# Optimization experiments

Measured on AMD Instinct MI355X. Metric: run time of the kernel, lower is better.

## Reference

```python
import jax, jax.numpy as jnp
import numpy as np

NUM_TOTAL = 150000
NUM_USER = 50000
NUM_ITEM = NUM_TOTAL - NUM_USER
D = 128
SOC_L = 2
CO_L = 2
NEG = 10
R = 0.7
E_SOC = 1600000
E_CO = 3200000
B = 512
MAX_UI = 64
MAX_IU = 50
W = 32
HOP = 3


def _sage_lgcn(x, src, dst, w, n, layers):
    # SAGEConv with edge-softmax weights over destination (LGCN 'mean' option).
    m = jax.lax.stop_gradient(jax.ops.segment_max(w, dst, num_segments=n))
    e = jnp.exp(w - m[dst])
    s = jax.ops.segment_sum(e, dst, num_segments=n)
    alpha = e / (s[dst] + 1e-16)
    for _ in range(layers):
        x = jax.ops.segment_sum(alpha[:, None] * x[src], dst, num_segments=n)
    return x  # LGCN.forward returns the last conv output (not the averaged sum)


def _sym_lgcn(x, src, dst, n, layers):
    # LGCConv: gcn_norm with added self-loops, symmetric D^-1/2 A D^-1/2.
    loop = jnp.arange(n)
    s2 = jnp.concatenate([src, loop])
    d2 = jnp.concatenate([dst, loop])
    deg = jax.ops.segment_sum(jnp.ones_like(d2, dtype=jnp.float32), d2, num_segments=n)
    dinv = jnp.where(deg > 0, deg ** -0.5, 0.0)
    ew = dinv[s2] * dinv[d2]
    for _ in range(layers):
        x = jax.ops.segment_sum(ew[:, None] * x[s2], d2, num_segments=n)
    return x


def _l2norm(x):
    return x / jnp.maximum(jnp.linalg.norm(x, axis=-1, keepdims=True), 1e-12)


def setup_inputs() -> dict:
    ks = jax.random.split(jax.random.key(0), 10)
    id_emb = 0.1 * jax.random.normal(ks[0], (NUM_TOTAL, D), jnp.float32)
    soc_id_emb = 0.1 * jax.random.normal(ks[1], (NUM_TOTAL, D), jnp.float32)
    soc_ext_weight = jax.random.uniform(ks[2], (E_SOC,), jnp.float32)
    soc_edge_index = jax.random.randint(ks[3], (2, E_SOC), 0, NUM_TOTAL)
    co_edge_index = jax.random.randint(ks[4], (2, E_CO), 0, NUM_TOTAL)
    uid = jax.random.randint(ks[5], (B,), 0, NUM_USER)
    pi = jax.random.randint(ks[9], (B,), NUM_USER, NUM_TOTAL)
    n_id = jnp.stack([uid, pi], axis=1)
    user_items = jax.random.randint(ks[6], (B, MAX_UI), 0, NUM_ITEM)
    item_users = jax.random.randint(ks[7], (NUM_ITEM, MAX_IU), 0, NUM_USER)
    walks = jax.random.randint(ks[8], (B, W, HOP), 0, NUM_TOTAL)
    return dict(id_emb=id_emb, soc_id_emb=soc_id_emb, soc_ext_weight=soc_ext_weight,
                soc_edge_index=soc_edge_index, co_edge_index=co_edge_index, n_id=n_id,
                user_items=user_items, item_users=item_users, walks=walks)


def reference(id_emb, soc_id_emb, soc_ext_weight, soc_edge_index, co_edge_index,
              n_id, user_items, item_users, walks):
    pi_id = n_id[:, 1]
    # two message-passing stacks
    soc_emb = _sage_lgcn(soc_id_emb, soc_edge_index[0], soc_edge_index[1],
                         soc_ext_weight, NUM_TOTAL, SOC_L)
    co_emb = _sym_lgcn(id_emb, co_edge_index[0], co_edge_index[1], NUM_TOTAL, CO_L)
    zero = jnp.zeros((1, D), id_emb.dtype)
    co_pad = jnp.concatenate([co_emb, zero], 0)
    soc_pad = jnp.concatenate([soc_emb, zero], 0)
    # vectorized per-user negative sampling: exclude interacted items, sample
    # NEG without replacement via top-k over masked uniform noise.
    rows = jnp.arange(B)[:, None]
    cols = jnp.where(user_items >= 0, user_items, 0)
    avail = jnp.ones((B, NUM_ITEM), jnp.int32).at[rows, cols].min(
        (user_items < 0).astype(jnp.int32))
    noise = jax.random.uniform(jax.random.key(42), (B, NUM_ITEM))
    scorez = jnp.where(avail > 0, noise, -1.0)
    _, neg_local = jax.lax.top_k(scorez, NEG)
    cand = jnp.concatenate([pi_id[:, None], neg_local + NUM_USER], axis=1)  # [B, 1+NEG]
    # item anchor soc embedding = mean of soc_emb over interacting users
    iu_idx = jnp.where(item_users >= 0, item_users, NUM_TOTAL)  # pad -> zero row
    cnt = (item_users >= 0).sum(-1, keepdims=True).astype(id_emb.dtype) + 1e-7
    anchor = soc_pad[iu_idx].sum(1) / cnt  # [NUM_ITEM, D]
    u_ref = jnp.concatenate([soc_emb[:NUM_USER], anchor, zero], 0)  # [NUM_TOTAL+1, D]
    co_n = _l2norm(co_pad)
    soc_n = _l2norm(u_ref)
    wk = walks.reshape(B, -1)  # [B, W*HOP]
    co_sim = (jnp.einsum('bcd,bwd->bcw', co_n[cand], co_n[wk]) + 1.0) * 0.5
    soc_sim = (jnp.einsum('bcd,bwd->bcw', soc_n[cand], soc_n[wk]) + 1.0) * 0.5
    return R * co_sim.mean(-1) + (1.0 - R) * soc_sim.mean(-1)  # [B, 1+NEG]
```

## Files before the change

kernel.cpp:

```cpp
#include <hip/hip_runtime.h>
#include <hip/hip_fp16.h>
#include <stdint.h>

#define NUM_TOTAL 150000
#define NUM_USER  50000
#define NUM_ITEM  100000
#define E_SOC 1600000
#define E_CO  3200000
#define BATCH 512
#define MAX_UI 64
#define MAX_IU 50
#define NWALK 96
#define NCAND 11
#define NB    586
#define NWG   192
#define PARTS 4
#define PIT   25000
#define PMW   784
#define SCAP  192
#define TH    8377900u

__device__ __forceinline__ uint32_t rotl32(uint32_t x, int r){ return (x<<r)|(x>>(32-r)); }

__device__ __forceinline__ void tf_core(uint32_t x0, uint32_t x1, uint32_t& o0, uint32_t& o1){
  const uint32_t k0 = 0u, k1 = 42u, k2 = 0u ^ 42u ^ 0x1BD11BDAu;
  x0 += k0; x1 += k1;
#define TF_R4(a,b,c,d) \
  x0+=x1; x1=rotl32(x1,a); x1^=x0; \
  x0+=x1; x1=rotl32(x1,b); x1^=x0; \
  x0+=x1; x1=rotl32(x1,c); x1^=x0; \
  x0+=x1; x1=rotl32(x1,d); x1^=x0;
  TF_R4(13,15,26,6)   x0+=k1; x1+=k2+1u;
  TF_R4(17,29,16,24)  x0+=k2; x1+=k0+2u;
  TF_R4(13,15,26,6)   x0+=k0; x1+=k1+3u;
  TF_R4(17,29,16,24)  x0+=k1; x1+=k2+4u;
  TF_R4(13,15,26,6)   x0+=k2; x1+=k0+5u;
#undef TF_R4
  o0 = x0; o1 = x1;
}

__device__ __forceinline__ uint32_t tf_bits(uint32_t j){
  uint32_t o0, o1;
  tf_core(0u, j, o0, o1);
  return o0 ^ o1;
}

__global__ __launch_bounds__(256) void pcountB_k(const int* __restrict__ socDst,
                                                 const int* __restrict__ coDst,
                                                 int chunkS, int chunkC,
                                                 int* __restrict__ cntMatS,
                                                 int* __restrict__ cntMatC){
  __shared__ int h[NB];
  int tid = threadIdx.x;
  bool isSoc = blockIdx.x < NWG;
  int wg = isSoc ? blockIdx.x : blockIdx.x - NWG;
  const int* dst = isSoc ? socDst : coDst;
  int E = isSoc ? E_SOC : E_CO;
  int chunk = isSoc ? chunkS : chunkC;
  int* cntMat = isSoc ? cntMatS : cntMatC;
  for (int i=tid; i<NB; i+=256) h[i]=0;
  __syncthreads();
  int lo = wg*chunk, hi = lo+chunk; if (hi > E) hi = E;
  for (int i=lo+tid; i<hi; i+=256) atomicAdd(&h[dst[i]>>8], 1);
  __syncthreads();
  for (int i=tid; i<NB; i+=256) cntMat[wg*NB + i] = h[i];
}

__global__ __launch_bounds__(1024) void pscan2_k(int* __restrict__ cntMatS, int* __restrict__ cntMatC,
                                                 int* __restrict__ bbaseS, int* __restrict__ bbaseC){
  __shared__ int sa[1024];
  int tid = threadIdx.x;
  int* cntMat = blockIdx.x ? cntMatC : cntMatS;
  int* bbase  = blockIdx.x ? bbaseC  : bbaseS;
  int E       = blockIdx.x ? E_CO    : E_SOC;
  int tot = 0;
  if (tid < NB){
    for (int wg=0; wg<NWG; ++wg) tot += cntMat[wg*NB + tid];
  }
  sa[tid] = tot;
  __syncthreads();
  for (int s=1; s<1024; s<<=1){
    int v = (tid>=s)?sa[tid-s]:0;
    __syncthreads();
    sa[tid] += v;
    __syncthreads();
  }
  if (tid < NB){
    int base = sa[tid] - tot;
    bbase[tid] = base;
    int run = base;
    for (int wg=0; wg<NWG; ++wg){
      int c = cntMat[wg*NB + tid];
      cntMat[wg*NB + tid] = run;
      run += c;
    }
  }
  if (tid == 0) bbase[NB] = E;
}

__global__ __launch_bounds__(256) void pplaceB_k(const int* __restrict__ socSrc,
        const int* __restrict__ socDst, const float* __restrict__ socWgt,
        const int* __restrict__ coSrc,  const int* __restrict__ coDst,
        const int* __restrict__ cntMatS, const int* __restrict__ cntMatC,
        unsigned long long* __restrict__ recS, unsigned int* __restrict__ recC,
        int chunkS, int chunkC){
  __shared__ int curx[NB];
  int tid = threadIdx.x;
  bool isSoc = blockIdx.x < NWG;
  int wg = isSoc ? blockIdx.x : blockIdx.x - NWG;
  const int* offMat = isSoc ? cntMatS : cntMatC;
  for (int i=tid; i<NB; i+=256) curx[i] = offMat[wg*NB + i];
  __syncthreads();
  if (isSoc){
    int lo = wg*chunkS, hi = lo+chunkS; if (hi > E_SOC) hi = E_SOC;
    for (int i=lo+tid; i<hi; i+=256){
      int d = socDst[i];
      int p = atomicAdd(&curx[d>>8], 1);
      recS[p] = ((unsigned long long)__float_as_uint(socWgt[i])<<32)
              | (unsigned)(((d&255)<<18) | socSrc[i]);
    }
  } else {
    int lo = wg*chunkC, hi = lo+chunkC; if (hi > E_CO) hi = E_CO;
    for (int i=lo+tid; i<hi; i+=256){
      int d = coDst[i];
      int p = atomicAdd(&curx[d>>8], 1);
      recC[p] = (unsigned)(((d&255)<<18) | coSrc[i]);
    }
  }
}

__global__ __launch_bounds__(256) void cscB_k(const unsigned long long* __restrict__ recS,
    const unsigned int* __restrict__ recC,
    const int* __restrict__ bbaseS, const int* __restrict__ bbaseC,
    int* __restrict__ socOff, int* __restrict__ socSrcS, float* __restrict__ socWS,
    int* __restrict__ coOff, int* __restrict__ coSrcS, float* __restrict__ dinv){
  __shared__ int cnt[256], basex[256], curx[256];
  int tid = threadIdx.x;
  bool isSoc = blockIdx.x < NB;
  int b = isSoc ? blockIdx.x : blockIdx.x - NB;
  const int* bbase = isSoc ? bbaseS : bbaseC;
  int lo = bbase[b], hi = bbase[b+1];
  cnt[tid] = 0;
  __syncthreads();
  if (isSoc){
    for (int i = lo + tid; i < hi; i += 256)
      atomicAdd(&cnt[(((unsigned)recS[i]) >> 18) & 255], 1);
  } else {
    for (int i = lo + tid; i < hi; i += 256)
      atomicAdd(&cnt[(recC[i] >> 18) & 255], 1);
  }
  __syncthreads();
  int c = cnt[tid];
  basex[tid] = c; __syncthreads();
  for (int s=1; s<256; s<<=1){
    int t = (tid>=s)?basex[tid-s]:0; __syncthreads();
    basex[tid]+=t; __syncthreads();
  }
  int excl = basex[tid]-c;
  int node = b*256+tid;
  int* off = isSoc ? socOff : coOff;
  if (node <= NUM_TOTAL) off[node] = lo + excl;
  basex[tid] = excl; curx[tid] = 0;
  __syncthreads();
  if (isSoc){
    for (int i = lo + tid; i < hi; i += 256){
      unsigned long long r = recS[i];
      unsigned lw = (unsigned)r;
      int dl = (lw>>18)&255;
      int p = lo + basex[dl] + atomicAdd(&curx[dl],1);
      socSrcS[p] = lw & 0x3FFFF;
      socWS[p] = __uint_as_float((unsigned)(r>>32));
    }
    __syncthreads();
    if (node < NUM_TOTAL && c > 0){
      int e0 = lo + basex[tid], e1 = e0 + c;
      float m = -3.402823466e+38f;
      for (int e=e0; e<e1; ++e) m = fmaxf(m, socWS[e]);
      float s = 0.f;
      for (int e=e0; e<e1; ++e) s += expf(socWS[e] - m);
      float inv = 1.0f / (s + 1e-16f);
      for (int e=e0; e<e1; ++e) socWS[e] = expf(socWS[e] - m) * inv;
    }
  } else {
    for (int i = lo + tid; i < hi; i += 256){
      unsigned r = recC[i];
      int dl = (r>>18)&255;
      int p = lo + basex[dl] + atomicAdd(&curx[dl],1);
      coSrcS[p] = r & 0x3FFFF;
    }
    if (node < NUM_TOTAL) dinv[node] = 1.0f / sqrtf((float)(c + 1));
  }
}

__global__ void f2h2_k(const float4* __restrict__ a, uint2* __restrict__ oa,
                       const float4* __restrict__ b, uint2* __restrict__ ob, int n4){
  int i = blockIdx.x*blockDim.x+threadIdx.x, st = gridDim.x*blockDim.x;
  for (; i<n4; i+=st){
    float4 va = a[i], vb = b[i];
    __half2 l = __float22half2_rn(make_float2(va.x,va.y));
    __half2 h = __float22half2_rn(make_float2(va.z,va.w));
    uint2 u; u.x = *(unsigned*)&l; u.y = *(unsigned*)&h;
    oa[i] = u;
    l = __float22half2_rn(make_float2(vb.x,vb.y));
    h = __float22half2_rn(make_float2(vb.z,vb.w));
    u.x = *(unsigned*)&l; u.y = *(unsigned*)&h;
    ob[i] = u;
  }
}

__global__ void agg_soc8_k(const __half2* __restrict__ x, __half2* __restrict__ y,
                           const int* __restrict__ off, const int* __restrict__ srcS,
                           const float* __restrict__ wE, int n){
  int gw = (blockIdx.x*blockDim.x + threadIdx.x) >> 6;
  int lane = threadIdx.x & 63;
  if (gw >= n) return;
  float ax = 0.f, ay = 0.f;
  int e = off[gw], e1 = off[gw+1];
  for (; e + 8 <= e1; e += 8){
    int s0=srcS[e],s1=srcS[e+1],s2=srcS[e+2],s3=srcS[e+3];
    int s4=srcS[e+4],s5=srcS[e+5],s6=srcS[e+6],s7=srcS[e+7];
    float a0=wE[e],a1=wE[e+1],a2=wE[e+2],a3=wE[e+3];
    float a4=wE[e+4],a5=wE[e+5],a6=wE[e+6],a7=wE[e+7];
    __half2 h0=x[(size_t)s0*64+lane], h1=x[(size_t)s1*64+lane];
    __half2 h2=x[(size_t)s2*64+lane], h3=x[(size_t)s3*64+lane];
    __half2 h4=x[(size_t)s4*64+lane], h5=x[(size_t)s5*64+lane];
    __half2 h6=x[(size_t)s6*64+lane], h7=x[(size_t)s7*64+lane];
    float2 f0=__half22float2(h0), f1=__half22float2(h1), f2=__half22float2(h2), f3=__half22float2(h3);
    float2 f4=__half22float2(h4), f5=__half22float2(h5), f6=__half22float2(h6), f7=__half22float2(h7);
    ax += a0*f0.x + a1*f1.x + a2*f2.x + a3*f3.x + a4*f4.x + a5*f5.x + a6*f6.x + a7*f7.x;
    ay += a0*f0.y + a1*f1.y + a2*f2.y + a3*f3.y + a4*f4.y + a5*f5.y + a6*f6.y + a7*f7.y;
  }
  for (; e < e1; ++e){
    int s = srcS[e]; float a = wE[e];
    float2 f = __half22float2(x[(size_t)s*64 + lane]);
    ax += a*f.x; ay += a*f.y;
  }
  y[(size_t)gw*64 + lane] = __float22half2_rn(make_float2(ax, ay));
}

__global__ void agg_co8_k(const __half2* __restrict__ x, __half2* __restrict__ y,
                          const int* __restrict__ off, const int* __restrict__ srcS,
                          const float* __restrict__ dinv, int n){
  int gw = (blockIdx.x*blockDim.x + threadIdx.x) >> 6;
  int lane = threadIdx.x & 63;
  if (gw >= n) return;
  float dv = dinv[gw];
  float2 fs = __half22float2(x[(size_t)gw*64 + lane]);
  float ax = dv*dv*fs.x, ay = dv*dv*fs.y;
  int e = off[gw], e1 = off[gw+1];
  for (; e + 8 <= e1; e += 8){
    int s0=srcS[e],s1=srcS[e+1],s2=srcS[e+2],s3=srcS[e+3];
    int s4=srcS[e+4],s5=srcS[e+5],s6=srcS[e+6],s7=srcS[e+7];
    float a0=dinv[s0]*dv,a1=dinv[s1]*dv,a2=dinv[s2]*dv,a3=dinv[s3]*dv;
    float a4=dinv[s4]*dv,a5=dinv[s5]*dv,a6=dinv[s6]*dv,a7=dinv[s7]*dv;
    __half2 h0=x[(size_t)s0*64+lane], h1=x[(size_t)s1*64+lane];
    __half2 h2=x[(size_t)s2*64+lane], h3=x[(size_t)s3*64+lane];
    __half2 h4=x[(size_t)s4*64+lane], h5=x[(size_t)s5*64+lane];
    __half2 h6=x[(size_t)s6*64+lane], h7=x[(size_t)s7*64+lane];
    float2 f0=__half22float2(h0), f1=__half22float2(h1), f2=__half22float2(h2), f3=__half22float2(h3);
    float2 f4=__half22float2(h4), f5=__half22float2(h5), f6=__half22float2(h6), f7=__half22float2(h7);
    ax += a0*f0.x + a1*f1.x + a2*f2.x + a3*f3.x + a4*f4.x + a5*f5.x + a6*f6.x + a7*f7.x;
    ay += a0*f0.y + a1*f1.y + a2*f2.y + a3*f3.y + a4*f4.y + a5*f5.y + a6*f6.y + a7*f7.y;
  }
  for (; e < e1; ++e){
    int s = srcS[e]; float a = dinv[s]*dv;
    float2 f = __half22float2(x[(size_t)s*64 + lane]);
    ax += a*f.x; ay += a*f.y;
  }
  y[(size_t)gw*64 + lane] = __float22half2_rn(make_float2(ax, ay));
}

__global__ void norm_h_k(__half2* __restrict__ x, int n){
  int gw = (blockIdx.x*blockDim.x + threadIdx.x) >> 6;
  int lane = threadIdx.x & 63;
  if (gw >= n) return;
  __half2* p = x + (size_t)gw*64;
  float2 v = __half22float2(p[lane]);
  float ss = v.x*v.x + v.y*v.y;
  #pragma unroll
  for (int s=32; s; s>>=1) ss += __shfl_xor(ss, s, 64);
  float sc = 1.0f / fmaxf(sqrtf(ss), 1e-12f);
  p[lane] = __float22half2_rn(make_float2(v.x*sc, v.y*sc));
}

__global__ void postA_k(__half2* __restrict__ coE, const __half2* __restrict__ socE,
                        const int* __restrict__ item_users, __half2* __restrict__ anch){
  int gw = (blockIdx.x*blockDim.x + threadIdx.x) >> 6;
  int lane = threadIdx.x & 63;
  if (gw < NUM_TOTAL){
    __half2* p = coE + (size_t)gw*64;
    float2 v = __half22float2(p[lane]);
    float ss = v.x*v.x + v.y*v.y;
    #pragma unroll
    for (int s=32; s; s>>=1) ss += __shfl_xor(ss, s, 64);
    float sc = 1.0f / fmaxf(sqrtf(ss), 1e-12f);
    p[lane] = __float22half2_rn(make_float2(v.x*sc, v.y*sc));
  } else {
    int it = gw - NUM_TOTAL;
    if (it >= NUM_ITEM) return;
    const int* us = item_users + (size_t)it*MAX_IU;
    float ax = 0.f, ay = 0.f;
    for (int k=0; k<MAX_IU; k+=10){
      int u0=us[k],u1=us[k+1],u2=us[k+2],u3=us[k+3],u4=us[k+4];
      int u5=us[k+5],u6=us[k+6],u7=us[k+7],u8=us[k+8],u9=us[k+9];
      __half2 h0=socE[(size_t)u0*64+lane], h1=socE[(size_t)u1*64+lane];
      __half2 h2=socE[(size_t)u2*64+lane], h3=socE[(size_t)u3*64+lane];
      __half2 h4=socE[(size_t)u4*64+lane], h5=socE[(size_t)u5*64+lane];
      __half2 h6=socE[(size_t)u6*64+lane], h7=socE[(size_t)u7*64+lane];
      __half2 h8=socE[(size_t)u8*64+lane], h9=socE[(size_t)u9*64+lane];
      float2 f0=__half22float2(h0), f1=__half22float2(h1), f2=__half22float2(h2);
      float2 f3=__half22float2(h3), f4=__half22float2(h4), f5=__half22float2(h5);
      float2 f6=__half22float2(h6), f7=__half22float2(h7), f8=__half22float2(h8);
      float2 f9=__half22float2(h9);
      ax += f0.x+f1.x+f2.x+f3.x+f4.x+f5.x+f6.x+f7.x+f8.x+f9.x;
      ay += f0.y+f1.y+f2.y+f3.y+f4.y+f5.y+f6.y+f7.y+f8.y+f9.y;
    }
    const float inv = 1.0f / (50.0f + 1e-7f);
    ax *= inv; ay *= inv;
    float ss = ax*ax + ay*ay;
    #pragma unroll
    for (int s=32; s; s>>=1) ss += __shfl_xor(ss, s, 64);
    float sc = 1.0f / fmaxf(sqrtf(ss), 1e-12f);
    anch[(size_t)it*64 + lane] = __float22half2_rn(make_float2(ax*sc, ay*sc));
  }
}

__global__ __launch_bounds__(256) void negA_k(const int* __restrict__ user_items,
                                              unsigned long long* __restrict__ surv,
                                              int* __restrict__ scnt){
  __shared__ unsigned int mask[PMW];
  __shared__ int lcnt;
  int blk = blockIdx.x;
  int row = blk >> 2, part = blk & 3;
  int base = part * PIT;
  int tid = threadIdx.x;
  for (int i=tid; i<PMW; i+=256) mask[i] = 0u;
  if (tid == 0) lcnt = 0;
  __syncthreads();
  if (tid < MAX_UI){
    int it = user_items[row*MAX_UI + tid];
    if (it >= base && it < base + PIT){
      int li = it - base;
      atomicOr(&mask[li>>5], 1u << (li & 31));
    }
  }
  __syncthreads();
  unsigned jbase = (unsigned)row * 100000u + (unsigned)base;
  for (int k = tid; k < PIT; k += 1024){
    int i1 = k + 256, i2 = k + 512, i3 = k + 768;
    uint32_t b0 = tf_bits(jbase + (unsigned)k);
    uint32_t b1 = tf_bits(jbase + (unsigned)(i1 < PIT ? i1 : k));
    uint32_t b2 = tf_bits(jbase + (unsigned)(i2 < PIT ? i2 : k));
    uint32_t b3 = tf_bits(jbase + (unsigned)(i3 < PIT ? i3 : k));
    uint32_t v0 = b0 >> 9, v1 = b1 >> 9, v2 = b2 >> 9, v3 = b3 >> 9;
    if (v0 >= TH && !((mask[k>>5] >> (k&31)) & 1u)){
      int p = atomicAdd(&lcnt, 1);
      if (p < SCAP)
        surv[(size_t)blk*SCAP + p] = ((unsigned long long)v0 << 32) | (unsigned)(~(unsigned)(base + k));
    }
    if (i1 < PIT && v1 >= TH && !((mask[i1>>5] >> (i1&31)) & 1u)){
      int p = atomicAdd(&lcnt, 1);
      if (p < SCAP)
        surv[(size_t)blk*SCAP + p] = ((unsigned long long)v1 << 32) | (unsigned)(~(unsigned)(base + i1));
    }
    if (i2 < PIT && v2 >= TH && !((mask[i2>>5] >> (i2&31)) & 1u)){
      int p = atomicAdd(&lcnt, 1);
      if (p < SCAP)
        surv[(size_t)blk*SCAP + p] = ((unsigned long long)v2 << 32) | (unsigned)(~(unsigned)(base + i2));
    }
    if (i3 < PIT && v3 >= TH && !((mask[i3>>5] >> (i3&31)) & 1u)){
      int p = atomicAdd(&lcnt, 1);
      if (p < SCAP)
        surv[(size_t)blk*SCAP + p] = ((unsigned long long)v3 << 32) | (unsigned)(~(unsigned)(base + i3));
    }
  }
  __syncthreads();
  if (tid == 0) scnt[blk] = (lcnt < SCAP) ? lcnt : SCAP;
}

__global__ __launch_bounds__(256) void negB_k(const unsigned long long* __restrict__ surv,
                                              const int* __restrict__ scnt,
                                              const int* __restrict__ user_items,
                                              const int* __restrict__ n_id,
                                              int* __restrict__ cand){
  __shared__ unsigned long long keys[PARTS*SCAP];
  __shared__ unsigned long long red[256];
  __shared__ int cnts[PARTS];
  __shared__ int uix[MAX_UI];
  int b = blockIdx.x, tid = threadIdx.x;
  if (tid < PARTS) cnts[tid] = scnt[b*PARTS + tid];
  for (int i=tid; i<PARTS*SCAP; i+=256) keys[i] = 0ull;
  __syncthreads();
  int o0 = 0, o1 = cnts[0], o2 = o1 + cnts[1], o3 = o2 + cnts[2];
  int total = o3 + cnts[3];
  if (tid < cnts[0]) keys[o0 + tid] = surv[(size_t)(b*PARTS+0)*SCAP + tid];
  if (tid < cnts[1]) keys[o1 + tid] = surv[(size_t)(b*PARTS+1)*SCAP + tid];
  if (tid < cnts[2]) keys[o2 + tid] = surv[(size_t)(b*PARTS+2)*SCAP + tid];
  if (tid < cnts[3]) keys[o3 + tid] = surv[(size_t)(b*PARTS+3)*SCAP + tid];
  __syncthreads();
  if (total >= 10){
    for (int r=0; r<10; ++r){
      unsigned long long m = 0ull;
      for (int i=tid; i<PARTS*SCAP; i+=256){ unsigned long long v = keys[i]; if (v > m) m = v; }
      red[tid] = m; __syncthreads();
      for (int s=128; s>0; s>>=1){
        if (tid < s && red[tid+s] > red[tid]) red[tid] = red[tid+s];
        __syncthreads();
      }
      unsigned long long win = red[0];
      if (tid == 0)
        cand[b*NCAND + 1 + r] = NUM_USER + (int)(~(unsigned)(win & 0xffffffffull));
      for (int i=tid; i<PARTS*SCAP; i+=256) if (keys[i] == win) keys[i] = 0ull;
      __syncthreads();
    }
  } else {
    if (tid < MAX_UI) uix[tid] = user_items[b*MAX_UI + tid];
    __syncthreads();
    unsigned long long prev = ~0ull;
    for (int r=0; r<10; ++r){
      unsigned long long m = 0ull;
      for (int i=tid; i<NUM_ITEM; i+=256){
        bool msk = false;
        for (int j=0; j<MAX_UI; ++j) if (uix[j] == i) msk = true;
        if (msk) continue;
        uint32_t v = tf_bits((unsigned)b*100000u + (unsigned)i) >> 9;
        unsigned long long key = ((unsigned long long)v << 32) | (unsigned)(~(unsigned)i);
        if (key < prev && key > m) m = key;
      }
      red[tid] = m; __syncthreads();
      for (int s=128; s>0; s>>=1){
        if (tid < s && red[tid+s] > red[tid]) red[tid] = red[tid+s];
        __syncthreads();
      }
      unsigned long long win = red[0];
      prev = win;
      if (tid == 0)
        cand[b*NCAND + 1 + r] = NUM_USER + (int)(~(unsigned)(win & 0xffffffffull));
      __syncthreads();
    }
  }
  if (tid == 0) cand[b*NCAND] = n_id[b*2 + 1];
}

__global__ void sim_h_k(const __half2* __restrict__ coN, const __half2* __restrict__ socU,
                        const __half2* __restrict__ socI, const int* __restrict__ cand,
                        const int* __restrict__ walks, float* __restrict__ out){
  int b = blockIdx.x;
  int lane = threadIdx.x;
  float scx=0.f, scy=0.f, ssx=0.f, ssy=0.f;
  for (int w=0; w<NWALK; w+=4){
    int i0 = walks[b*NWALK + w],   i1 = walks[b*NWALK + w+1];
    int i2 = walks[b*NWALK + w+2], i3 = walks[b*NWALK + w+3];
    __half2 c0 = coN[(size_t)i0*64 + lane], c1 = coN[(size_t)i1*64 + lane];
    __half2 c2 = coN[(size_t)i2*64 + lane], c3 = coN[(size_t)i3*64 + lane];
    const __half2* p0 = (i0 < NUM_USER) ? socU + (size_t)i0*64 : socI + (size_t)(i0-NUM_USER)*64;
    const __half2* p1 = (i1 < NUM_USER) ? socU + (size_t)i1*64 : socI + (size_t)(i1-NUM_USER)*64;
    const __half2* p2 = (i2 < NUM_USER) ? socU + (size_t)i2*64 : socI + (size_t)(i2-NUM_USER)*64;
    const __half2* p3 = (i3 < NUM_USER) ? socU + (size_t)i3*64 : socI + (size_t)(i3-NUM_USER)*64;
    __half2 s0 = p0[lane], s1 = p1[lane], s2 = p2[lane], s3 = p3[lane];
    float2 fc0 = __half22float2(c0), fc1 = __half22float2(c1);
    float2 fc2 = __half22float2(c2), fc3 = __half22float2(c3);
    float2 fs0 = __half22float2(s0), fs1 = __half22float2(s1);
    float2 fs2 = __half22float2(s2), fs3 = __half22float2(s3);
    scx += fc0.x + fc1.x + fc2.x + fc3.x;
    scy += fc0.y + fc1.y + fc2.y + fc3.y;
    ssx += fs0.x + fs1.x + fs2.x + fs3.x;
    ssy += fs0.y + fs1.y + fs2.y + fs3.y;
  }
  for (int c=0; c<NCAND; ++c){
    int idx = cand[b*NCAND + c];
    float2 cv = __half22float2(coN[(size_t)idx*64 + lane]);
    float2 sv = __half22float2(socI[(size_t)(idx - NUM_USER)*64 + lane]);
    float dco = cv.x*scx + cv.y*scy;
    float dso = sv.x*ssx + sv.y*ssy;
    #pragma unroll
    for (int s=32; s; s>>=1){
      dco += __shfl_xor(dco, s, 64);
      dso += __shfl_xor(dso, s, 64);
    }
    if (lane == 0){
      float com = 0.5f + 0.5f*(dco / 96.0f);
      float som = 0.5f + 0.5f*(dso / 96.0f);
      out[b*NCAND + c] = 0.7f*com + 0.3f*som;
    }
  }
}

extern "C" void kernel_launch(void* const* d_in, const int* in_sizes, int n_in,
                              void* d_out, int out_size, void* d_ws, size_t ws_size,
                              hipStream_t stream){
  (void)in_sizes; (void)n_in; (void)out_size; (void)ws_size;
  const float* id_emb     = (const float*)d_in[0];
  const float* soc_id_emb = (const float*)d_in[1];
  const float* soc_w      = (const float*)d_in[2];
  const int*   soc_ei     = (const int*)d_in[3];
  const int*   co_ei      = (const int*)d_in[4];
  const int*   n_id       = (const int*)d_in[5];
  const int*   user_items = (const int*)d_in[6];
  const int*   item_users = (const int*)d_in[7];
  const int*   walks      = (const int*)d_in[8];
  float* out = (float*)d_out;

  char* w = (char*)d_ws;
  size_t cur = 0;
  auto take = [&](size_t bytes)->void*{
    void* p = w + cur;
    cur = (cur + bytes + 255) & ~(size_t)255;
    return p;
  };
  __half2* socId16 = (__half2*)take((size_t)NUM_TOTAL*64*4);
  __half2* id16    = (__half2*)take((size_t)NUM_TOTAL*64*4);
  __half2* t16     = (__half2*)take((size_t)NUM_TOTAL*64*4);
  __half2* soc16   = (__half2*)take((size_t)NUM_TOTAL*64*4);
  __half2* co16    = (__half2*)take((size_t)NUM_TOTAL*64*4);
  int*   socOff  = (int*)take((size_t)(NUM_TOTAL+1)*4);
  int*   coOff   = (int*)take((size_t)(NUM_TOTAL+1)*4);
  float* dinv    = (float*)take((size_t)NUM_TOTAL*4);
  int*   socSrcS = (int*)take((size_t)E_SOC*4);
  float* socWS   = (float*)take((size_t)E_SOC*4);
  int*   coSrcS  = (int*)take((size_t)E_CO*4);
  int*   cntMatS = (int*)take((size_t)NWG*NB*4);
  int*   cntMatC = (int*)take((size_t)NWG*NB*4);
  int*   bbaseS  = (int*)take((size_t)(NB+1)*4);
  int*   bbaseC  = (int*)take((size_t)(NB+1)*4);
  unsigned long long* surv = (unsigned long long*)take((size_t)BATCH*PARTS*SCAP*8);
  int*   scnt    = (int*)take((size_t)BATCH*PARTS*4);
  int*   cand    = (int*)take((size_t)BATCH*NCAND*4);

  unsigned long long* recS = (unsigned long long*)t16;
  unsigned int*       recC = (unsigned int*)((char*)t16 + (size_t)E_SOC*8);

  __half2* anch16 = socId16;

  const int T = 256;
  const int chunkS = (E_SOC + NWG - 1) / NWG;
  const int chunkC = (E_CO  + NWG - 1) / NWG;

  pcountB_k<<<2*NWG, T, 0, stream>>>(soc_ei + E_SOC, co_ei + E_CO, chunkS, chunkC, cntMatS, cntMatC);
  pscan2_k<<<2, 1024, 0, stream>>>(cntMatS, cntMatC, bbaseS, bbaseC);
  pplaceB_k<<<2*NWG, T, 0, stream>>>(soc_ei, soc_ei + E_SOC, soc_w,
                                     co_ei, co_ei + E_CO,
                                     cntMatS, cntMatC, recS, recC, chunkS, chunkC);
  cscB_k<<<2*NB, T, 0, stream>>>(recS, recC, bbaseS, bbaseC,
                                 socOff, socSrcS, socWS, coOff, coSrcS, dinv);

  negA_k<<<BATCH*PARTS, T, 0, stream>>>(user_items, surv, scnt);

  f2h2_k<<<2048, T, 0, stream>>>((const float4*)soc_id_emb, (uint2*)socId16,
                                 (const float4*)id_emb,     (uint2*)id16, NUM_TOTAL*32);

  int aggGrid = (NUM_TOTAL + 3) / 4;
  agg_soc8_k<<<aggGrid, T, 0, stream>>>(socId16, soc16, socOff, socSrcS, socWS, NUM_TOTAL);
  agg_soc8_k<<<aggGrid, T, 0, stream>>>(soc16,   t16,   socOff, socSrcS, socWS, NUM_TOTAL);
  agg_co8_k <<<aggGrid, T, 0, stream>>>(id16,    co16,  coOff,  coSrcS,  dinv,  NUM_TOTAL);
  agg_co8_k <<<aggGrid, T, 0, stream>>>(co16,    id16,  coOff,  coSrcS,  dinv,  NUM_TOTAL);

  __half2* socE = t16;
  __half2* coE  = id16;

  postA_k<<<(2*NUM_TOTAL - NUM_USER + 3)/4, T, 0, stream>>>(coE, socE, item_users, anch16);
  norm_h_k<<<(NUM_USER + 3)/4, T, 0, stream>>>(socE, NUM_USER);

  negB_k<<<BATCH, T, 0, stream>>>(surv, scnt, user_items, n_id, cand);
  sim_h_k<<<BATCH, 64, 0, stream>>>(coE, socE, anch16, cand, walks, out);
}
```

Baseline: 983.6 us.

## Parallelize bucket-offset scan across wavefronts and fuse negative sampling with fp16 conversion

The count matrix is transposed to a bucket-major layout. The serial per-thread scan over 192 workgroups in a 2-block kernel is replaced by three kernels: a wavefront-per-bucket total, a small block scan, and a wavefront-per-bucket prefix that writes placement offsets. Separately, the negative-candidate survivor kernel and the fp32-to-fp16 embedding conversion are merged into one launch so their blocks can run concurrently. This adds two extra launches for the scan and a heterogeneous fused kernel.

```diff
diff --git a/kernel.cpp b/kernel.cpp
--- a/kernel.cpp
+++ b/kernel.cpp
@@ -63,39 +63,64 @@
   int lo = wg*chunk, hi = lo+chunk; if (hi > E) hi = E;
   for (int i=lo+tid; i<hi; i+=256) atomicAdd(&h[dst[i]>>8], 1);
   __syncthreads();
-  for (int i=tid; i<NB; i+=256) cntMat[wg*NB + i] = h[i];
-}
-
-__global__ __launch_bounds__(1024) void pscan2_k(int* __restrict__ cntMatS, int* __restrict__ cntMatC,
+  for (int i=tid; i<NB; i+=256) cntMat[(size_t)i*NWG + wg] = h[i];
+}
+
+__global__ void btot2_k(const int* __restrict__ cntMatS, const int* __restrict__ cntMatC,
+                        int* __restrict__ totS, int* __restrict__ totC){
+  int g = (blockIdx.x*blockDim.x + threadIdx.x) >> 6;
+  int lane = threadIdx.x & 63;
+  if (g >= 2*NB) return;
+  bool isSoc = g < NB;
+  int b = isSoc ? g : g - NB;
+  const int* row = (isSoc ? cntMatS : cntMatC) + (size_t)b*NWG;
+  int s = row[lane*3] + row[lane*3+1] + row[lane*3+2];
+  #pragma unroll
+  for (int d=32; d; d>>=1) s += __shfl_xor(s, d, 64);
+  if (lane == 0) (isSoc ? totS : totC)[b] = s;
+}
+
+__global__ __launch_bounds__(1024) void bscan2_k(const int* __restrict__ totS, const int* __restrict__ totC,
                                                  int* __restrict__ bbaseS, int* __restrict__ bbaseC){
   __shared__ int sa[1024];
   int tid = threadIdx.x;
-  int* cntMat = blockIdx.x ? cntMatC : cntMatS;
-  int* bbase  = blockIdx.x ? bbaseC  : bbaseS;
-  int E       = blockIdx.x ? E_CO    : E_SOC;
-  int tot = 0;
-  if (tid < NB){
-    for (int wg=0; wg<NWG; ++wg) tot += cntMat[wg*NB + tid];
-  }
-  sa[tid] = tot;
+  const int* tot = blockIdx.x ? totC : totS;
+  int* bbase     = blockIdx.x ? bbaseC : bbaseS;
+  int E          = blockIdx.x ? E_CO   : E_SOC;
+  int v = (tid < NB) ? tot[tid] : 0;
+  sa[tid] = v;
   __syncthreads();
   for (int s=1; s<1024; s<<=1){
-    int v = (tid>=s)?sa[tid-s]:0;
-    __syncthreads();
-    sa[tid] += v;
-    __syncthreads();
-  }
-  if (tid < NB){
-    int base = sa[tid] - tot;
-    bbase[tid] = base;
-    int run = base;
-    for (int wg=0; wg<NWG; ++wg){
-      int c = cntMat[wg*NB + tid];
-      cntMat[wg*NB + tid] = run;
-      run += c;
-    }
-  }
+    int t = (tid>=s)?sa[tid-s]:0;
+    __syncthreads();
+    sa[tid] += t;
+    __syncthreads();
+  }
+  if (tid < NB) bbase[tid] = sa[tid] - v;
   if (tid == 0) bbase[NB] = E;
+}
+
+__global__ void wgpfx2_k(int* __restrict__ cntMatS, int* __restrict__ cntMatC,
+                         const int* __restrict__ bbaseS, const int* __restrict__ bbaseC){
+  int g = (blockIdx.x*blockDim.x + threadIdx.x) >> 6;
+  int lane = threadIdx.x & 63;
+  if (g >= 2*NB) return;
+  bool isSoc = g < NB;
+  int b = isSoc ? g : g - NB;
+  int* row = (isSoc ? cntMatS : cntMatC) + (size_t)b*NWG;
+  int base = (isSoc ? bbaseS : bbaseC)[b];
+  int v0 = row[lane*3], v1 = row[lane*3+1], v2 = row[lane*3+2];
+  int s = v0 + v1 + v2;
+  int x = s;
+  #pragma unroll
+  for (int d=1; d<64; d<<=1){
+    int t = __shfl_up(x, d, 64);
+    if (lane >= d) x += t;
+  }
+  int excl = x - s;
+  row[lane*3]   = base + excl;
+  row[lane*3+1] = base + excl + v0;
+  row[lane*3+2] = base + excl + v0 + v1;
 }
 
 __global__ __launch_bounds__(256) void pplaceB_k(const int* __restrict__ socSrc,
@@ -109,7 +134,7 @@
   bool isSoc = blockIdx.x < NWG;
   int wg = isSoc ? blockIdx.x : blockIdx.x - NWG;
   const int* offMat = isSoc ? cntMatS : cntMatC;
-  for (int i=tid; i<NB; i+=256) curx[i] = offMat[wg*NB + i];
+  for (int i=tid; i<NB; i+=256) curx[i] = offMat[(size_t)i*NWG + wg];
   __syncthreads();
   if (isSoc){
     int lo = wg*chunkS, hi = lo+chunkS; if (hi > E_SOC) hi = E_SOC;
@@ -192,19 +217,73 @@
   }
 }
 
-__global__ void f2h2_k(const float4* __restrict__ a, uint2* __restrict__ oa,
-                       const float4* __restrict__ b, uint2* __restrict__ ob, int n4){
-  int i = blockIdx.x*blockDim.x+threadIdx.x, st = gridDim.x*blockDim.x;
-  for (; i<n4; i+=st){
-    float4 va = a[i], vb = b[i];
-    __half2 l = __float22half2_rn(make_float2(va.x,va.y));
-    __half2 h = __float22half2_rn(make_float2(va.z,va.w));
-    uint2 u; u.x = *(unsigned*)&l; u.y = *(unsigned*)&h;
-    oa[i] = u;
-    l = __float22half2_rn(make_float2(vb.x,vb.y));
-    h = __float22half2_rn(make_float2(vb.z,vb.w));
-    u.x = *(unsigned*)&l; u.y = *(unsigned*)&h;
-    ob[i] = u;
+__global__ __launch_bounds__(256) void negAf2h_k(const int* __restrict__ user_items,
+        unsigned long long* __restrict__ surv, int* __restrict__ scnt,
+        const float4* __restrict__ fa, uint2* __restrict__ oa,
+        const float4* __restrict__ fb, uint2* __restrict__ ob, int n4){
+  __shared__ unsigned int mask[PMW];
+  __shared__ int lcnt;
+  int tid = threadIdx.x;
+  if (blockIdx.x < BATCH*PARTS){
+    int blk = blockIdx.x;
+    int row = blk >> 2, part = blk & 3;
+    int base = part * PIT;
+    for (int i=tid; i<PMW; i+=256) mask[i] = 0u;
+    if (tid == 0) lcnt = 0;
+    __syncthreads();
+    if (tid < MAX_UI){
+      int it = user_items[row*MAX_UI + tid];
+      if (it >= base && it < base + PIT){
+        int li = it - base;
+        atomicOr(&mask[li>>5], 1u << (li & 31));
+      }
+    }
+    __syncthreads();
+    unsigned jbase = (unsigned)row * 100000u + (unsigned)base;
+    for (int k = tid; k < PIT; k += 1024){
+      int i1 = k + 256, i2 = k + 512, i3 = k + 768;
+      uint32_t b0 = tf_bits(jbase + (unsigned)k);
+      uint32_t b1 = tf_bits(jbase + (unsigned)(i1 < PIT ? i1 : k));
+      uint32_t b2 = tf_bits(jbase + (unsigned)(i2 < PIT ? i2 : k));
+      uint32_t b3 = tf_bits(jbase + (unsigned)(i3 < PIT ? i3 : k));
+      uint32_t v0 = b0 >> 9, v1 = b1 >> 9, v2 = b2 >> 9, v3 = b3 >> 9;
+      if (v0 >= TH && !((mask[k>>5] >> (k&31)) & 1u)){
+        int p = atomicAdd(&lcnt, 1);
+        if (p < SCAP)
+          surv[(size_t)blk*SCAP + p] = ((unsigned long long)v0 << 32) | (unsigned)(~(unsigned)(base + k));
+      }
+      if (i1 < PIT && v1 >= TH && !((mask[i1>>5] >> (i1&31)) & 1u)){
+        int p = atomicAdd(&lcnt, 1);
+        if (p < SCAP)
+          surv[(size_t)blk*SCAP + p] = ((unsigned long long)v1 << 32) | (unsigned)(~(unsigned)(base + i1));
+      }
+      if (i2 < PIT && v2 >= TH && !((mask[i2>>5] >> (i2&31)) & 1u)){
+        int p = atomicAdd(&lcnt, 1);
+        if (p < SCAP)
+          surv[(size_t)blk*SCAP + p] = ((unsigned long long)v2 << 32) | (unsigned)(~(unsigned)(base + i2));
+      }
+      if (i3 < PIT && v3 >= TH && !((mask[i3>>5] >> (i3&31)) & 1u)){
+        int p = atomicAdd(&lcnt, 1);
+        if (p < SCAP)
+          surv[(size_t)blk*SCAP + p] = ((unsigned long long)v3 << 32) | (unsigned)(~(unsigned)(base + i3));
+      }
+    }
+    __syncthreads();
+    if (tid == 0) scnt[blk] = (lcnt < SCAP) ? lcnt : SCAP;
+  } else {
+    int i = (int)(blockIdx.x - BATCH*PARTS)*256 + tid;
+    int st = 2048*256;
+    for (; i<n4; i+=st){
+      float4 va = fa[i], vb = fb[i];
+      __half2 l = __float22half2_rn(make_float2(va.x,va.y));
+      __half2 h = __float22half2_rn(make_float2(va.z,va.w));
+      uint2 u; u.x = *(unsigned*)&l; u.y = *(unsigned*)&h;
+      oa[i] = u;
+      l = __float22half2_rn(make_float2(vb.x,vb.y));
+      h = __float22half2_rn(make_float2(vb.z,vb.w));
+      u.x = *(unsigned*)&l; u.y = *(unsigned*)&h;
+      ob[i] = u;
+    }
   }
 }
 
@@ -325,59 +404,6 @@
   }
 }
 
-__global__ __launch_bounds__(256) void negA_k(const int* __restrict__ user_items,
-                                              unsigned long long* __restrict__ surv,
-                                              int* __restrict__ scnt){
-  __shared__ unsigned int mask[PMW];
-  __shared__ int lcnt;
-  int blk = blockIdx.x;
-  int row = blk >> 2, part = blk & 3;
-  int base = part * PIT;
-  int tid = threadIdx.x;
-  for (int i=tid; i<PMW; i+=256) mask[i] = 0u;
-  if (tid == 0) lcnt = 0;
-  __syncthreads();
-  if (tid < MAX_UI){
-    int it = user_items[row*MAX_UI + tid];
-    if (it >= base && it < base + PIT){
-      int li = it - base;
-      atomicOr(&mask[li>>5], 1u << (li & 31));
-    }
-  }
-  __syncthreads();
-  unsigned jbase = (unsigned)row * 100000u + (unsigned)base;
-  for (int k = tid; k < PIT; k += 1024){
-    int i1 = k + 256, i2 = k + 512, i3 = k + 768;
-    uint32_t b0 = tf_bits(jbase + (unsigned)k);
-    uint32_t b1 = tf_bits(jbase + (unsigned)(i1 < PIT ? i1 : k));
-    uint32_t b2 = tf_bits(jbase + (unsigned)(i2 < PIT ? i2 : k));
-    uint32_t b3 = tf_bits(jbase + (unsigned)(i3 < PIT ? i3 : k));
-    uint32_t v0 = b0 >> 9, v1 = b1 >> 9, v2 = b2 >> 9, v3 = b3 >> 9;
-    if (v0 >= TH && !((mask[k>>5] >> (k&31)) & 1u)){
-      int p = atomicAdd(&lcnt, 1);
-      if (p < SCAP)
-        surv[(size_t)blk*SCAP + p] = ((unsigned long long)v0 << 32) | (unsigned)(~(unsigned)(base + k));
-    }
-    if (i1 < PIT && v1 >= TH && !((mask[i1>>5] >> (i1&31)) & 1u)){
-      int p = atomicAdd(&lcnt, 1);
-      if (p < SCAP)
-        surv[(size_t)blk*SCAP + p] = ((unsigned long long)v1 << 32) | (unsigned)(~(unsigned)(base + i1));
-    }
-    if (i2 < PIT && v2 >= TH && !((mask[i2>>5] >> (i2&31)) & 1u)){
-      int p = atomicAdd(&lcnt, 1);
-      if (p < SCAP)
-        surv[(size_t)blk*SCAP + p] = ((unsigned long long)v2 << 32) | (unsigned)(~(unsigned)(base + i2));
-    }
-    if (i3 < PIT && v3 >= TH && !((mask[i3>>5] >> (i3&31)) & 1u)){
-      int p = atomicAdd(&lcnt, 1);
-      if (p < SCAP)
-        surv[(size_t)blk*SCAP + p] = ((unsigned long long)v3 << 32) | (unsigned)(~(unsigned)(base + i3));
-    }
-  }
-  __syncthreads();
-  if (tid == 0) scnt[blk] = (lcnt < SCAP) ? lcnt : SCAP;
-}
-
 __global__ __launch_bounds__(256) void negB_k(const unsigned long long* __restrict__ surv,
                                               const int* __restrict__ scnt,
                                               const int* __restrict__ user_items,
@@ -523,6 +549,8 @@
   int*   cntMatC = (int*)take((size_t)NWG*NB*4);
   int*   bbaseS  = (int*)take((size_t)(NB+1)*4);
   int*   bbaseC  = (int*)take((size_t)(NB+1)*4);
+  int*   totS    = (int*)take((size_t)NB*4);
+  int*   totC    = (int*)take((size_t)NB*4);
   unsigned long long* surv = (unsigned long long*)take((size_t)BATCH*PARTS*SCAP*8);
   int*   scnt    = (int*)take((size_t)BATCH*PARTS*4);
   int*   cand    = (int*)take((size_t)BATCH*NCAND*4);
@@ -537,16 +565,18 @@
   const int chunkC = (E_CO  + NWG - 1) / NWG;
 
   pcountB_k<<<2*NWG, T, 0, stream>>>(soc_ei + E_SOC, co_ei + E_CO, chunkS, chunkC, cntMatS, cntMatC);
-  pscan2_k<<<2, 1024, 0, stream>>>(cntMatS, cntMatC, bbaseS, bbaseC);
+  int scanGrid = (2*NB*64 + T - 1) / T;
+  btot2_k<<<scanGrid, T, 0, stream>>>(cntMatS, cntMatC, totS, totC);
+  bscan2_k<<<2, 1024, 0, stream>>>(totS, totC, bbaseS, bbaseC);
+  wgpfx2_k<<<scanGrid, T, 0, stream>>>(cntMatS, cntMatC, bbaseS, bbaseC);
   pplaceB_k<<<2*NWG, T, 0, stream>>>(soc_ei, soc_ei + E_SOC, soc_w,
                                      co_ei, co_ei + E_CO,
                                      cntMatS, cntMatC, recS, recC, chunkS, chunkC);
   cscB_k<<<2*NB, T, 0, stream>>>(recS, recC, bbaseS, bbaseC,
                                  socOff, socSrcS, socWS, coOff, coSrcS, dinv);
 
-  negA_k<<<BATCH*PARTS, T, 0, stream>>>(user_items, surv, scnt);
-
-  f2h2_k<<<2048, T, 0, stream>>>((const float4*)soc_id_emb, (uint2*)socId16,
+  negAf2h_k<<<BATCH*PARTS + 2048, T, 0, stream>>>(user_items, surv, scnt,
+                                 (const float4*)soc_id_emb, (uint2*)socId16,
                                  (const float4*)id_emb,     (uint2*)id16, NUM_TOTAL*32);
 
   int aggGrid = (NUM_TOTAL + 3) / 4;
```

Measured after the change: 951.0 us, median of 2. 3.3% less time.
